# Kernel optimization log

Measured on AMD Instinct MI355X. Metric: run time of the kernel, lower is better.

Reference implementation:

```python
import jax, jax.numpy as jnp
import numpy as np

N_ENT = 15000  # entity id range; also used for relation ids in this synthetic setup

def _triple_key(h, r, t):
    # Unique int64 key per (h, r, t) triple; max ~15000^3 < 2^63.
    return (h * N_ENT + r) * N_ENT + t

def setup_inputs() -> dict:
    key = jax.random.key(0)
    k1, k2, k3, k4 = jax.random.split(key, 4)
    Q, N = 100000, 10000000
    heads = jax.random.randint(k1, (Q,), 0, N_ENT, dtype=jnp.int64)
    rels = jax.random.randint(k2, (Q,), 0, N_ENT, dtype=jnp.int64)
    tails = jax.random.randint(k3, (Q,), 0, N_ENT, dtype=jnp.int64)
    data = jax.random.randint(k4, (3, N), 0, N_ENT, dtype=jnp.int64)
    return {"heads": heads, "rels": rels, "tails": tails, "data": data}

def reference(heads, rels, tails, data) -> jnp.ndarray:
    # Faithful to PerfeCT.forward: response[i] = 1 iff (heads[i], rels[i], tails[i])
    # appears as a row of data.T; output = 10 * (response - 0.5).
    data_keys = jnp.sort(_triple_key(data[0], data[1], data[2]))  # [N]
    q_keys = _triple_key(heads, rels, tails)                       # [Q]
    idx = jnp.searchsorted(data_keys, q_keys)
    idx = jnp.clip(idx, 0, data_keys.shape[0] - 1)
    member = (data_keys[idx] == q_keys).astype(jnp.float32)        # [Q]
    return 10.0 * (member - 0.5)
```

## Files before the change

kernel.cpp:

```cpp
#include <hip/hip_runtime.h>
#include <stdint.h>


#define EMPTY64     0xFFFFFFFFFFFFFFFFULL
#define BLOOM_WORDS 16384u
#define BLOOM_MASK  (BLOOM_WORDS - 1u)

typedef unsigned int       v4u   __attribute__((ext_vector_type(4)));
typedef unsigned long long v2u64 __attribute__((ext_vector_type(2)));

__device__ __forceinline__ uint32_t key32(uint32_t h, uint32_t r, uint32_t t) {
    return (h * 15000u + r) * 15000u + t;
}

__device__ __forceinline__ uint64_t mix64(uint64_t x) {
    x ^= x >> 30; x *= 0xbf58476d1ce4e5b9ULL;
    x ^= x >> 27; x *= 0x94d049bb133111ebULL;
    x ^= x >> 31;
    return x;
}

__global__ void clear_ws(uint4* __restrict__ table4, unsigned n_table4,
                         uint4* __restrict__ bloom4, unsigned n_bloom4) {
    unsigned i = blockIdx.x * blockDim.x + threadIdx.x;
    if (i < n_table4) table4[i] = make_uint4(~0u, ~0u, ~0u, ~0u);
    if (i < n_bloom4) bloom4[i] = make_uint4(0u, 0u, 0u, 0u);
}

__global__ void insert_queries(const int* __restrict__ heads,
                               const int* __restrict__ rels,
                               const int* __restrict__ tails,
                               unsigned long long* __restrict__ table,
                               unsigned tmask,
                               uint32_t* __restrict__ g_bloom,
                               float* __restrict__ out,
                               int Q) {
    int i = blockIdx.x * blockDim.x + threadIdx.x;
    if (i >= Q) return;
    out[i] = -5.0f;
    uint32_t key = key32((uint32_t)heads[i], (uint32_t)rels[i], (uint32_t)tails[i]);
    uint64_t mix = mix64(key);
    uint32_t bm = (1u << ((mix >> 46) & 31u)) | (1u << ((mix >> 51) & 31u));
    atomicOr(&g_bloom[(mix >> 32) & BLOOM_MASK], bm);
    uint64_t entry = (uint64_t)key | ((uint64_t)(unsigned)i << 32);
    unsigned slot = ((unsigned)mix & (tmask >> 1)) << 1;
    for (unsigned step = 0; step <= tmask; ++step) {
        if (atomicCAS(&table[slot], EMPTY64, (unsigned long long)entry) == EMPTY64) break;
        slot = (slot + 1u) & tmask;
    }
}

__device__ __forceinline__ void probe_pairs(uint32_t key, unsigned b,
                                            const v2u64* __restrict__ tb,
                                            unsigned bmask,
                                            float* __restrict__ out) {
    for (unsigned step = 0; step <= bmask; ++step) {
        v2u64 e = tb[b];
        bool le = (e.x == EMPTY64), he = (e.y == EMPTY64);
        if (!le && (uint32_t)e.x == key) out[e.x >> 32] = 5.0f;
        if (!he && (uint32_t)e.y == key) out[e.y >> 32] = 5.0f;
        if (le || he) return;
        b = (b + 1u) & bmask;
    }
}

__global__ __launch_bounds__(1024, 8)
void scan_data(const int* __restrict__ data, int N,
               const unsigned long long* __restrict__ table,
               unsigned tmask,
               const uint32_t* __restrict__ g_bloom,
               float* __restrict__ out) {
    __shared__ uint32_t bloom[BLOOM_WORDS];
    {
        const uint4* src = (const uint4*)g_bloom;
        uint4* dst = (uint4*)bloom;
        for (unsigned w = threadIdx.x; w < BLOOM_WORDS / 4; w += blockDim.x)
            dst[w] = src[w];
    }
    __syncthreads();

    const unsigned tid    = blockIdx.x * blockDim.x + threadIdx.x;
    const unsigned stride = gridDim.x * blockDim.x;
    const unsigned bmask  = tmask >> 1;
    const v2u64* tb = (const v2u64*)table;

    if ((N & 3) == 0) {
        const int nq = N >> 2;
        const v4u* h4 = (const v4u*)data;
        const v4u* r4 = (const v4u*)(data + (size_t)N);
        const v4u* t4 = (const v4u*)(data + 2 * (size_t)N);
        for (unsigned q = tid; q < (unsigned)nq; q += stride) {
            v4u h = __builtin_nontemporal_load(&h4[q]);
            v4u r = __builtin_nontemporal_load(&r4[q]);
            v4u t = __builtin_nontemporal_load(&t4[q]);

            uint32_t k0 = key32(h.x, r.x, t.x);
            uint32_t k1 = key32(h.y, r.y, t.y);
            uint32_t k2 = key32(h.z, r.z, t.z);
            uint32_t k3 = key32(h.w, r.w, t.w);
            uint64_t m0 = mix64(k0), m1 = mix64(k1), m2 = mix64(k2), m3 = mix64(k3);

            uint32_t w0 = bloom[(uint32_t)(m0 >> 32) & BLOOM_MASK];
            uint32_t w1 = bloom[(uint32_t)(m1 >> 32) & BLOOM_MASK];
            uint32_t w2 = bloom[(uint32_t)(m2 >> 32) & BLOOM_MASK];
            uint32_t w3 = bloom[(uint32_t)(m3 >> 32) & BLOOM_MASK];
            uint32_t bm0 = (1u << ((m0 >> 46) & 31u)) | (1u << ((m0 >> 51) & 31u));
            uint32_t bm1 = (1u << ((m1 >> 46) & 31u)) | (1u << ((m1 >> 51) & 31u));
            uint32_t bm2 = (1u << ((m2 >> 46) & 31u)) | (1u << ((m2 >> 51) & 31u));
            uint32_t bm3 = (1u << ((m3 >> 46) & 31u)) | (1u << ((m3 >> 51) & 31u));

            bool d0 = (w0 & bm0) != bm0;
            bool d1 = (w1 & bm1) != bm1;
            bool d2 = (w2 & bm2) != bm2;
            bool d3 = (w3 & bm3) != bm3;
            unsigned b0 = (unsigned)m0 & bmask;
            unsigned b1 = (unsigned)m1 & bmask;
            unsigned b2 = (unsigned)m2 & bmask;
            unsigned b3 = (unsigned)m3 & bmask;

            for (unsigned g = 0; (g <= bmask) && !(d0 && d1 && d2 && d3); ++g) {
                v2u64 e0, e1, e2, e3;
                if (!d0) e0 = tb[b0];
                if (!d1) e1 = tb[b1];
                if (!d2) e2 = tb[b2];
                if (!d3) e3 = tb[b3];
#define EVAL_PAIR(e, k, b, d)                                              \
                if (!(d)) {                                                \
                    bool le = ((e).x == EMPTY64), he = ((e).y == EMPTY64); \
                    if (!le && (uint32_t)(e).x == (k)) out[(e).x >> 32] = 5.0f; \
                    if (!he && (uint32_t)(e).y == (k)) out[(e).y >> 32] = 5.0f; \
                    if (le || he) (d) = true;                              \
                    else (b) = ((b) + 1u) & bmask;                         \
                }
                EVAL_PAIR(e0, k0, b0, d0)
                EVAL_PAIR(e1, k1, b1, d1)
                EVAL_PAIR(e2, k2, b2, d2)
                EVAL_PAIR(e3, k3, b3, d3)
#undef EVAL_PAIR
            }
        }
    } else {
        for (unsigned i = tid; i < (unsigned)N; i += stride) {
            uint32_t key = key32((uint32_t)data[i],
                                 (uint32_t)data[(size_t)N + i],
                                 (uint32_t)data[2 * (size_t)N + i]);
            uint64_t mix = mix64(key);
            uint32_t w  = bloom[(uint32_t)(mix >> 32) & BLOOM_MASK];
            uint32_t bm = (1u << ((mix >> 46) & 31u)) | (1u << ((mix >> 51) & 31u));
            if ((w & bm) != bm) continue;
            probe_pairs(key, (unsigned)mix & bmask, tb, bmask, out);
        }
    }
}

extern "C" void kernel_launch(void* const* d_in, const int* in_sizes, int n_in,
                              void* d_out, int out_size, void* d_ws, size_t ws_size,
                              hipStream_t stream) {
    const int* heads = (const int*)d_in[0];
    const int* rels  = (const int*)d_in[1];
    const int* tails = (const int*)d_in[2];
    const int* data  = (const int*)d_in[3];
    float* out = (float*)d_out;

    const int Q = in_sizes[0];
    const int N = in_sizes[3] / 3;

    size_t cap = 1ull << 18;
    if (cap * 8 + BLOOM_WORDS * 4 > ws_size) cap = 1ull << 17;
    if (cap * 8 + BLOOM_WORDS * 4 > ws_size) return;
    unsigned tmask = (unsigned)(cap - 1);
    unsigned long long* table = (unsigned long long*)d_ws;
    uint32_t* g_bloom = (uint32_t*)((char*)d_ws + cap * 8);

    {
        unsigned n_table4 = (unsigned)(cap / 2);
        unsigned n_bloom4 = BLOOM_WORDS / 4;
        unsigned n = n_table4 > n_bloom4 ? n_table4 : n_bloom4;
        dim3 block(256), grid((n + 255) / 256);
        clear_ws<<<grid, block, 0, stream>>>((uint4*)table, n_table4,
                                             (uint4*)g_bloom, n_bloom4);
    }
    {
        dim3 block(256), grid((Q + 255) / 256);
        insert_queries<<<grid, block, 0, stream>>>(heads, rels, tails, table, tmask,
                                                   g_bloom, out, Q);
    }
    {
        dim3 block(1024), grid(512);
        scan_data<<<grid, block, 0, stream>>>(data, N, table, tmask, g_bloom, out);
    }
}
```

Before: 212.1 us.

## Process eight keys per thread with speculative two-bucket probe prefetch

The scan loop now loads eight data elements per thread instead of four. For each key that passes the bloom filter it issues loads for two consecutive hash buckets up front, then falls back to a generic probe loop only for long chains. Block size drops from 1024 to 512 and the launch bounds change to match, which halves the total thread count while doubling the work per thread. The aim is more memory-level parallelism per thread and fewer probe loop iterations. The cost is higher register pressure and a speculative second bucket load that may be wasted.

```diff
diff --git a/kernel.cpp b/kernel.cpp
--- a/kernel.cpp
+++ b/kernel.cpp
@@ -64,7 +64,7 @@
     }
 }
 
-__global__ __launch_bounds__(1024, 8)
+__global__ __launch_bounds__(512, 4)
 void scan_data(const int* __restrict__ data, int N,
                const unsigned long long* __restrict__ table,
                unsigned tmask,
@@ -85,58 +85,96 @@
     const v2u64* tb = (const v2u64*)table;
 
     if ((N & 3) == 0) {
-        const int nq = N >> 2;
+        const unsigned nq4 = (unsigned)(N >> 2);
+        const unsigned nch = nq4 >> 1;
         const v4u* h4 = (const v4u*)data;
         const v4u* r4 = (const v4u*)(data + (size_t)N);
         const v4u* t4 = (const v4u*)(data + 2 * (size_t)N);
-        for (unsigned q = tid; q < (unsigned)nq; q += stride) {
-            v4u h = __builtin_nontemporal_load(&h4[q]);
-            v4u r = __builtin_nontemporal_load(&r4[q]);
-            v4u t = __builtin_nontemporal_load(&t4[q]);
-
-            uint32_t k0 = key32(h.x, r.x, t.x);
-            uint32_t k1 = key32(h.y, r.y, t.y);
-            uint32_t k2 = key32(h.z, r.z, t.z);
-            uint32_t k3 = key32(h.w, r.w, t.w);
-            uint64_t m0 = mix64(k0), m1 = mix64(k1), m2 = mix64(k2), m3 = mix64(k3);
-
-            uint32_t w0 = bloom[(uint32_t)(m0 >> 32) & BLOOM_MASK];
-            uint32_t w1 = bloom[(uint32_t)(m1 >> 32) & BLOOM_MASK];
-            uint32_t w2 = bloom[(uint32_t)(m2 >> 32) & BLOOM_MASK];
-            uint32_t w3 = bloom[(uint32_t)(m3 >> 32) & BLOOM_MASK];
-            uint32_t bm0 = (1u << ((m0 >> 46) & 31u)) | (1u << ((m0 >> 51) & 31u));
-            uint32_t bm1 = (1u << ((m1 >> 46) & 31u)) | (1u << ((m1 >> 51) & 31u));
-            uint32_t bm2 = (1u << ((m2 >> 46) & 31u)) | (1u << ((m2 >> 51) & 31u));
-            uint32_t bm3 = (1u << ((m3 >> 46) & 31u)) | (1u << ((m3 >> 51) & 31u));
-
-            bool d0 = (w0 & bm0) != bm0;
-            bool d1 = (w1 & bm1) != bm1;
-            bool d2 = (w2 & bm2) != bm2;
-            bool d3 = (w3 & bm3) != bm3;
-            unsigned b0 = (unsigned)m0 & bmask;
-            unsigned b1 = (unsigned)m1 & bmask;
-            unsigned b2 = (unsigned)m2 & bmask;
-            unsigned b3 = (unsigned)m3 & bmask;
-
-            for (unsigned g = 0; (g <= bmask) && !(d0 && d1 && d2 && d3); ++g) {
-                v2u64 e0, e1, e2, e3;
-                if (!d0) e0 = tb[b0];
-                if (!d1) e1 = tb[b1];
-                if (!d2) e2 = tb[b2];
-                if (!d3) e3 = tb[b3];
-#define EVAL_PAIR(e, k, b, d)                                              \
-                if (!(d)) {                                                \
-                    bool le = ((e).x == EMPTY64), he = ((e).y == EMPTY64); \
-                    if (!le && (uint32_t)(e).x == (k)) out[(e).x >> 32] = 5.0f; \
-                    if (!he && (uint32_t)(e).y == (k)) out[(e).y >> 32] = 5.0f; \
-                    if (le || he) (d) = true;                              \
-                    else (b) = ((b) + 1u) & bmask;                         \
+
+        for (unsigned c = tid; c < nch; c += stride) {
+            v4u h0 = __builtin_nontemporal_load(&h4[2 * c]);
+            v4u r0 = __builtin_nontemporal_load(&r4[2 * c]);
+            v4u t0 = __builtin_nontemporal_load(&t4[2 * c]);
+            v4u h1 = __builtin_nontemporal_load(&h4[2 * c + 1]);
+            v4u r1 = __builtin_nontemporal_load(&r4[2 * c + 1]);
+            v4u t1 = __builtin_nontemporal_load(&t4[2 * c + 1]);
+
+            uint32_t k[8];
+            k[0] = key32(h0.x, r0.x, t0.x); k[1] = key32(h0.y, r0.y, t0.y);
+            k[2] = key32(h0.z, r0.z, t0.z); k[3] = key32(h0.w, r0.w, t0.w);
+            k[4] = key32(h1.x, r1.x, t1.x); k[5] = key32(h1.y, r1.y, t1.y);
+            k[6] = key32(h1.z, r1.z, t1.z); k[7] = key32(h1.w, r1.w, t1.w);
+
+            bool d[8]; unsigned b[8];
+#pragma unroll
+            for (int j = 0; j < 8; ++j) {
+                uint64_t m  = mix64(k[j]);
+                uint32_t w  = bloom[(uint32_t)(m >> 32) & BLOOM_MASK];
+                uint32_t bm = (1u << ((m >> 46) & 31u)) | (1u << ((m >> 51) & 31u));
+                d[j] = (w & bm) != bm;
+                b[j] = (unsigned)m & bmask;
+            }
+
+            v2u64 eA[8], eB[8];
+#pragma unroll
+            for (int j = 0; j < 8; ++j) if (!d[j]) {
+                eA[j] = tb[b[j]];
+                eB[j] = tb[(b[j] + 1u) & bmask];
+            }
+#pragma unroll
+            for (int j = 0; j < 8; ++j) if (!d[j]) {
+                v2u64 e = eA[j];
+                bool le = (e.x == EMPTY64), he = (e.y == EMPTY64);
+                if (!le && (uint32_t)e.x == k[j]) out[e.x >> 32] = 5.0f;
+                if (!he && (uint32_t)e.y == k[j]) out[e.y >> 32] = 5.0f;
+                if (le || he) {
+                    d[j] = true;
+                } else {
+                    e = eB[j];
+                    le = (e.x == EMPTY64); he = (e.y == EMPTY64);
+                    if (!le && (uint32_t)e.x == k[j]) out[e.x >> 32] = 5.0f;
+                    if (!he && (uint32_t)e.y == k[j]) out[e.y >> 32] = 5.0f;
+                    if (le || he) d[j] = true;
+                    else          b[j] = (b[j] + 2u) & bmask;
                 }
-                EVAL_PAIR(e0, k0, b0, d0)
-                EVAL_PAIR(e1, k1, b1, d1)
-                EVAL_PAIR(e2, k2, b2, d2)
-                EVAL_PAIR(e3, k3, b3, d3)
-#undef EVAL_PAIR
+            }
+
+            bool any = false;
+#pragma unroll
+            for (int j = 0; j < 8; ++j) any = any || !d[j];
+            if (any) {
+                for (unsigned g = 0; g <= bmask; ++g) {
+                    v2u64 e[8];
+#pragma unroll
+                    for (int j = 0; j < 8; ++j) if (!d[j]) e[j] = tb[b[j]];
+#pragma unroll
+                    for (int j = 0; j < 8; ++j) if (!d[j]) {
+                        bool le = (e[j].x == EMPTY64), he = (e[j].y == EMPTY64);
+                        if (!le && (uint32_t)e[j].x == k[j]) out[e[j].x >> 32] = 5.0f;
+                        if (!he && (uint32_t)e[j].y == k[j]) out[e[j].y >> 32] = 5.0f;
+                        if (le || he) d[j] = true;
+                        else          b[j] = (b[j] + 1u) & bmask;
+                    }
+                    bool a2 = false;
+#pragma unroll
+                    for (int j = 0; j < 8; ++j) a2 = a2 || !d[j];
+                    if (!a2) break;
+                }
+            }
+        }
+
+        if ((nq4 & 1u) && tid == 0) {
+            unsigned gq = nq4 - 1u;
+            v4u h = h4[gq], r = r4[gq], t = t4[gq];
+            uint32_t kk[4] = { key32(h.x, r.x, t.x), key32(h.y, r.y, t.y),
+                               key32(h.z, r.z, t.z), key32(h.w, r.w, t.w) };
+#pragma unroll
+            for (int j = 0; j < 4; ++j) {
+                uint64_t m  = mix64(kk[j]);
+                uint32_t w  = bloom[(uint32_t)(m >> 32) & BLOOM_MASK];
+                uint32_t bm = (1u << ((m >> 46) & 31u)) | (1u << ((m >> 51) & 31u));
+                if ((w & bm) == bm)
+                    probe_pairs(kk[j], (unsigned)m & bmask, tb, bmask, out);
             }
         }
     } else {
@@ -186,7 +224,7 @@
                                                    g_bloom, out, Q);
     }
     {
-        dim3 block(1024), grid(512);
+        dim3 block(512), grid(512);
         scan_data<<<grid, block, 0, stream>>>(data, N, table, tmask, g_bloom, out);
     }
 }
```

Result: slower. 231.6 us (+9.2%).
